# Kernel tuning notes

Measured on AMD Instinct MI355X. Metric: run time of the kernel, lower is better.

Reference implementation:

```python
import jax, jax.numpy as jnp
import numpy as np

N, IN_DIM, HID, HEADS, OUT = 4096, 512, 256, 2, 40
LN_EPS = 1e-5


def setup_inputs() -> dict:
    key = jax.random.key(0)
    ks = jax.random.split(key, 12)
    s_in = 1.0 / np.sqrt(IN_DIM)
    s_o = 1.0 / np.sqrt(2 * HID)
    adj = jax.random.randint(ks[0], (HEADS, N, N), 0, 2).astype(jnp.float32)
    h = jax.random.normal(ks[1], (N, IN_DIM), dtype=jnp.float32)
    Wq = jax.random.uniform(ks[2], (HEADS, IN_DIM, HID), minval=-s_in, maxval=s_in)
    bq = jax.random.uniform(ks[3], (HEADS, HID), minval=-s_in, maxval=s_in)
    Wk = jax.random.uniform(ks[4], (HEADS, IN_DIM, HID), minval=-s_in, maxval=s_in)
    bk = jax.random.uniform(ks[5], (HEADS, HID), minval=-s_in, maxval=s_in)
    Wv = jax.random.uniform(ks[6], (HEADS, IN_DIM, HID), minval=-s_in, maxval=s_in)
    bv = jax.random.uniform(ks[7], (HEADS, HID), minval=-s_in, maxval=s_in)
    Wo = jax.random.uniform(ks[8], (2 * HID, IN_DIM), minval=-s_o, maxval=s_o)
    bo = jax.random.uniform(ks[9], (IN_DIM,), minval=-s_o, maxval=s_o)
    gamma = jnp.ones((IN_DIM,), jnp.float32)
    beta = jnp.zeros((IN_DIM,), jnp.float32)
    Wp = jax.random.uniform(ks[10], (IN_DIM, OUT), minval=-s_in, maxval=s_in)
    bp = jax.random.uniform(ks[11], (OUT,), minval=-s_in, maxval=s_in)
    return dict(adj=adj, h=h, Wq=Wq, bq=bq, Wk=Wk, bk=bk, Wv=Wv, bv=bv,
                Wo=Wo, bo=bo, gamma=gamma, beta=beta, Wp=Wp, bp=bp)


def reference(adj, h, Wq, bq, Wk, bk, Wv, bv, Wo, bo, gamma, beta, Wp, bp):
    # Per-head projections, vectorized over the head axis. [H, N, D]
    Q = jnp.einsum('ni,hid->hnd', h, Wq) + bq[:, None, :]
    K = jnp.einsum('ni,hid->hnd', h, Wk) + bk[:, None, :]
    V = jnp.einsum('ni,hid->hnd', h, Wv) + bv[:, None, :]
    # Dense QK^T, elementwise-multiplied (not -inf masked) by per-head adjacency.
    scores = jnp.einsum('hnd,hmd->hnm', Q, K) * adj          # [H, N, N]
    attn = jax.nn.softmax(scores, axis=-1)
    X = jnp.einsum('hnm,hmd->hnd', attn, V)                  # [H, N, D]
    # cat([X0, X1], dim=1) -> [N, H*D]
    X_final = jnp.transpose(X, (1, 0, 2)).reshape(N, HEADS * HID)
    z = X_final @ Wo + bo                                    # [N, IN_DIM]
    mu = jnp.mean(z, axis=-1, keepdims=True)
    var = jnp.var(z, axis=-1, keepdims=True)
    M = (z - mu) * jax.lax.rsqrt(var + LN_EPS) * gamma + beta
    return jax.nn.softmax(M @ Wp + bp, axis=1)               # [N, OUT]
```

## Files before the change

kernel.cpp:

```cpp
#include <hip/hip_runtime.h>
#include <hip/hip_bf16.h>

#define N_TOK 4096
#define D_IN  512
#define D_HID 256
#define N_OUT 40

typedef _Float16 half8 __attribute__((ext_vector_type(8)));
typedef _Float16 half4 __attribute__((ext_vector_type(4)));
typedef float    f32x4 __attribute__((ext_vector_type(4)));

__device__ __forceinline__ void async_copy16(const _Float16* g, _Float16* l) {
  __builtin_amdgcn_global_load_lds(
      (const __attribute__((address_space(1))) unsigned int*)(g),
      (__attribute__((address_space(3))) unsigned int*)(l), 16, 0, 0);
}

__device__ __forceinline__ void transpose_tile(const float* __restrict__ src, int in_ncols,
                                               _Float16* __restrict__ dst, int out_ncols,
                                               int i0, int d0, float* lds )
{
  int tid = threadIdx.x;
  int l15 = tid & 15, l4 = tid >> 4;
#pragma unroll
  for (int p = 0; p < 4; p++) {
    int ii = p * 16 + l4;
    float4 x = *(const float4*)(src + (size_t)(i0 + ii) * in_ncols + d0 + l15 * 4);
    lds[(l15 * 4 + 0) * 65 + ii] = x.x;
    lds[(l15 * 4 + 1) * 65 + ii] = x.y;
    lds[(l15 * 4 + 2) * 65 + ii] = x.z;
    lds[(l15 * 4 + 3) * 65 + ii] = x.w;
  }
  __syncthreads();
  int dd = tid >> 2, chunk = tid & 3;
  half8 o0, o1;
#pragma unroll
  for (int j = 0; j < 8; j++) o0[j] = (_Float16)lds[dd * 65 + chunk * 16 + j];
#pragma unroll
  for (int j = 0; j < 8; j++) o1[j] = (_Float16)lds[dd * 65 + chunk * 16 + 8 + j];
  *(half8*)(dst + (size_t)(d0 + dd) * out_ncols + i0 + chunk * 16) = o0;
  *(half8*)(dst + (size_t)(d0 + dd) * out_ncols + i0 + chunk * 16 + 8) = o1;
}

__global__ void prep_kernel(const float* __restrict__ h, const float* __restrict__ Wq,
                            const float* __restrict__ Wk, const float* __restrict__ Wv,
                            const float* __restrict__ Wo, const float* __restrict__ Wp,
                            _Float16* __restrict__ h16, _Float16* __restrict__ Wqt,
                            _Float16* __restrict__ Wkt, _Float16* __restrict__ Wvt,
                            _Float16* __restrict__ Wot, _Float16* __restrict__ Wpt)
{
  __shared__ float lds[64 * 65];
  int b = blockIdx.x, tid = threadIdx.x;
  if (b < 1024) {
    int base = b * 2048 + tid * 8;
    float4 x0 = *(const float4*)(h + base);
    float4 x1 = *(const float4*)(h + base + 4);
    half8 o;
    o[0]=(_Float16)x0.x; o[1]=(_Float16)x0.y; o[2]=(_Float16)x0.z; o[3]=(_Float16)x0.w;
    o[4]=(_Float16)x1.x; o[5]=(_Float16)x1.y; o[6]=(_Float16)x1.z; o[7]=(_Float16)x1.w;
    *(half8*)(h16 + base) = o;
  } else if (b < 1216) {
    int t = b - 1024;
    int mat = t >> 5;
    int m = mat >> 1, head = mat & 1;
    const float* W = (m==0 ? Wq : (m==1 ? Wk : Wv)) + head * (D_IN * D_HID);
    _Float16* Wt   = (m==0 ? Wqt : (m==1 ? Wkt : Wvt)) + head * (D_IN * D_HID);
    int tt = t & 31;
    int i0 = (tt >> 2) * 64, d0 = (tt & 3) * 64;
    transpose_tile(W, D_HID, Wt, D_IN, i0, d0, lds);
  } else if (b < 1280) {
    int t = b - 1216;
    int i0 = (t >> 3) * 64, d0 = (t & 7) * 64;
    transpose_tile(Wo, D_IN, Wot, D_IN, i0, d0, lds);
  } else {
    int blk = b - 1280;
    int idx = blk * 1024 + tid * 4;
    int j = idx >> 9, i = idx & 511;
    half4 o;
#pragma unroll
    for (int u = 0; u < 4; u++)
      o[u] = (j < N_OUT) ? (_Float16)Wp[(i + u) * N_OUT + j] : (_Float16)0.f;
    *(half4*)(Wpt + j * D_IN + i) = o;
  }
}

__global__ __launch_bounds__(256, 2) void proj_kernel(
    const _Float16* __restrict__ h16, const _Float16* __restrict__ W6 ,
    const _Float16* __restrict__ Wvt,
    const float* __restrict__ bq, const float* __restrict__ bk,
    const float* __restrict__ bv,
    _Float16* __restrict__ Q16, _Float16* __restrict__ K16,
    _Float16* __restrict__ VT16)
{
  __shared__ __align__(16) _Float16 Atile[128 * 64];
  __shared__ __align__(16) _Float16 Btile[128 * 64];

  int b = blockIdx.x;
  int tid = threadIdx.x, w = tid >> 6, lane = tid & 63, quad = lane >> 4, cL = lane & 15;
  int wr = w >> 1, wc = w & 1;

  const _Float16 *Asrc, *Bsrc;
  int isV;
  int m0 = 0, n0 = 0, head = 0, mh = 0;
  if (b < 256) {
    isV = 0;
    m0 = (b >> 3) * 128;
    int ct = b & 7;
    mh = ct >> 1;
    n0 = (ct & 1) * 128;
    Asrc = h16 + (size_t)m0 * D_IN;
    Bsrc = W6 + (size_t)(ct * 128) * D_IN;
  } else {
    isV = 1;
    int t = b - 256;
    head = t >> 6;
    int tt = t & 63;
    m0 = (tt >> 5) * 128;
    n0 = (tt & 31) * 128;
    Asrc = Wvt + (size_t)head * (D_HID * D_IN) + (size_t)m0 * D_IN;
    Bsrc = h16 + (size_t)n0 * D_IN;
  }

  const f32x4 z4 = {0.f, 0.f, 0.f, 0.f};
  f32x4 acc[4][4];
#pragma unroll
  for (int i = 0; i < 4; i++)
#pragma unroll
    for (int j = 0; j < 4; j++) acc[i][j] = z4;

  int r8 = lane >> 3, chs = (lane & 7) ^ r8;

  for (int kc = 0; kc < 8; kc++) {
    __syncthreads();
#pragma unroll
    for (int g = 0; g < 4; g++) {
      int row = (w * 4 + g) * 8 + r8;
      async_copy16(Asrc + (size_t)row * D_IN + kc * 64 + chs * 8, Atile + (w * 4 + g) * 512);
      async_copy16(Bsrc + (size_t)row * D_IN + kc * 64 + chs * 8, Btile + (w * 4 + g) * 512);
    }
    __syncthreads();
#pragma unroll
    for (int kk = 0; kk < 2; kk++) {
      int ch = ((kk * 4 + quad) ^ (cL & 7)) * 8;
      half8 a[4], bf[4];
#pragma unroll
      for (int mt = 0; mt < 4; mt++)
        a[mt] = *(const half8*)(Atile + (wr * 64 + mt * 16 + cL) * 64 + ch);
#pragma unroll
      for (int nt = 0; nt < 4; nt++)
        bf[nt] = *(const half8*)(Btile + (wc * 64 + nt * 16 + cL) * 64 + ch);
#pragma unroll
      for (int mt = 0; mt < 4; mt++)
#pragma unroll
        for (int nt = 0; nt < 4; nt++)
          acc[mt][nt] = __builtin_amdgcn_mfma_f32_16x16x32_f16(a[mt], bf[nt], acc[mt][nt], 0, 0, 0);
    }
  }

  if (!isV) {
    _Float16* Out = (mh < 2 ? Q16 + (size_t)mh * (N_TOK * D_HID)
                            : K16 + (size_t)(mh - 2) * (N_TOK * D_HID));
    const float* bias = (mh < 2 ? bq + mh * D_HID : bk + (mh - 2) * D_HID);
#pragma unroll
    for (int mt = 0; mt < 4; mt++) {
      int row = m0 + wr * 64 + mt * 16 + quad * 4;
#pragma unroll
      for (int nt = 0; nt < 4; nt++) {
        int colg = n0 + wc * 64 + nt * 16 + cL;
        float bb = bias[colg];
#pragma unroll
        for (int reg = 0; reg < 4; reg++)
          Out[(size_t)(row + reg) * D_HID + colg] = (_Float16)(acc[mt][nt][reg] + bb);
      }
    }
  } else {
    _Float16* VTh = VT16 + (size_t)head * (N_TOK * D_HID);
    const float* bvh = bv + head * D_HID;
#pragma unroll
    for (int mt = 0; mt < 4; mt++) {
      int d0r = m0 + wr * 64 + mt * 16 + quad * 4;
      float bvv[4];
#pragma unroll
      for (int reg = 0; reg < 4; reg++) bvv[reg] = bvh[d0r + reg];
#pragma unroll
      for (int nt = 0; nt < 4; nt++) {
        int tok = n0 + wc * 64 + nt * 16 + cL;
#pragma unroll
        for (int reg = 0; reg < 4; reg++)
          VTh[(size_t)(d0r + reg) * N_TOK + tok] = (_Float16)(acc[mt][nt][reg] + bvv[reg]);
      }
    }
  }
}

__global__ __launch_bounds__(512, 2) void attn_kernel(
    const float* __restrict__ adj, const _Float16* __restrict__ Q16,
    const _Float16* __restrict__ K16, const _Float16* __restrict__ VT16,
    _Float16* __restrict__ Opart, float* __restrict__ Mpart, float* __restrict__ Lpart)
{
  __shared__ __align__(16) _Float16 Kt[2][64 * 256];
  __shared__ __align__(16) _Float16 Vt[2][256 * 64];
  __shared__ __align__(16) _Float16 Pbuf[8 * 16 * 72];

  int b = blockIdx.x;
  int head = (b >> 2) & 1;
  int gs = b & 3;
  int q0 = (b >> 3) * 128;

  int tid = threadIdx.x;
  int w = tid >> 6, lane = tid & 63, quad = lane >> 4, cL = lane & 15;

  const _Float16* Qh = Q16 + head * (N_TOK * D_HID);
  const _Float16* Kh = K16 + head * (N_TOK * D_HID);
  const _Float16* Vh = VT16 + head * (N_TOK * D_HID);
  const float* adjh = adj + (size_t)head * N_TOK * N_TOK;

  int qrow = q0 + w * 16;
  int nstart = gs * 1024;
  const f32x4 z4 = {0.f, 0.f, 0.f, 0.f};

  half8 qf[8];
#pragma unroll
  for (int t = 0; t < 8; t++)
    qf[t] = *(const half8*)(Qh + (qrow + cL) * D_HID + t * 32 + quad * 8);

  f32x4 acc[16];
#pragma unroll
  for (int i = 0; i < 16; i++) acc[i] = z4;
  float m_i[4] = {-1e30f, -1e30f, -1e30f, -1e30f};
  float l_i[4] = {0.f, 0.f, 0.f, 0.f};

  _Float16* pb = Pbuf + w * (16 * 72);

  const float* adjR[4];
#pragma unroll
  for (int reg = 0; reg < 4; reg++)
    adjR[reg] = adjh + (size_t)(qrow + quad * 4 + reg) * N_TOK + nstart + cL;

  int l5 = lane >> 5, l31 = lane & 31;
  int l3 = lane >> 3, l7 = lane & 7;

  auto stageK = [&](int it, _Float16* dst) {
    int n0 = nstart + it * 64;
#pragma unroll
    for (int i = 0; i < 4; i++) {
      int g = w * 4 + i;
      int rK = 2 * g + l5;
      int cK = l31 ^ (rK & 7);
      async_copy16(Kh + (size_t)(n0 + rK) * D_HID + cK * 8, dst + g * 512);
    }
  };
  auto stageV = [&](int it, _Float16* dst) {
    int n0 = nstart + it * 64;
#pragma unroll
    for (int i = 0; i < 4; i++) {
      int g = w * 4 + i;
      int rV = g * 8 + l3;
      int cV = l7 ^ (rV & 7);
      async_copy16(Vh + (size_t)rV * N_TOK + n0 + cV * 8, dst + g * 512);
    }
  };
  auto loadAdj = [&](int it, float (&av)[4][4]) {
#pragma unroll
    for (int reg = 0; reg < 4; reg++)
#pragma unroll
      for (int ct = 0; ct < 4; ct++)
        av[reg][ct] = __builtin_nontemporal_load(adjR[reg] + it * 64 + ct * 16);
  };

  auto body = [&](int it, const _Float16* KC, const _Float16* VC,
                  _Float16* KN, _Float16* VN,
                  float (&avC)[4][4], float (&avN)[4][4]) {
    if (it + 1 < 16) {
      stageK(it + 1, KN);
      stageV(it + 1, VN);
      loadAdj(it + 1, avN);
    }

    f32x4 s[4];
#pragma unroll
    for (int ct = 0; ct < 4; ct++) s[ct] = z4;
#pragma unroll
    for (int t = 0; t < 8; t++) {
#pragma unroll
      for (int ct = 0; ct < 4; ct++) {
        int rK = ct * 16 + cL;
        int ck = (t * 4 + quad) ^ (rK & 7);
        half8 kf = *(const half8*)(KC + rK * 256 + ck * 8);
        s[ct] = __builtin_amdgcn_mfma_f32_16x16x32_f16(qf[t], kf, s[ct], 0, 0, 0);
      }
    }

    float alpha[4];
#pragma unroll
    for (int reg = 0; reg < 4; reg++) {
#pragma unroll
      for (int ct = 0; ct < 4; ct++) s[ct][reg] *= avC[reg][ct];
      float mx = fmaxf(fmaxf(s[0][reg], s[1][reg]), fmaxf(s[2][reg], s[3][reg]));
#pragma unroll
      for (int msk = 1; msk < 16; msk <<= 1) mx = fmaxf(mx, __shfl_xor(mx, msk, 16));
      float mnew = fmaxf(m_i[reg], mx);
      alpha[reg] = __expf(m_i[reg] - mnew);
      m_i[reg] = mnew;
      float rs = 0.f;
#pragma unroll
      for (int ct = 0; ct < 4; ct++) {
        float p = __expf(s[ct][reg] - mnew);
        s[ct][reg] = p;
        rs += p;
      }
#pragma unroll
      for (int msk = 1; msk < 16; msk <<= 1) rs += __shfl_xor(rs, msk, 16);
      l_i[reg] = l_i[reg] * alpha[reg] + rs;
    }

#pragma unroll
    for (int reg = 0; reg < 4; reg++)
#pragma unroll
      for (int ct = 0; ct < 4; ct++)
        pb[(quad * 4 + reg) * 72 + ct * 16 + cL] = (_Float16)s[ct][reg];

    if (__any(alpha[0] * alpha[1] * alpha[2] * alpha[3] != 1.0f)) {
#pragma unroll
      for (int dt = 0; dt < 16; dt++)
#pragma unroll
        for (int reg = 0; reg < 4; reg++)
          acc[dt][reg] *= alpha[reg];
    }

    half8 pf0 = *(const half8*)(pb + cL * 72 + quad * 8);
    half8 pf1 = *(const half8*)(pb + cL * 72 + 32 + quad * 8);
#pragma unroll
    for (int dt = 0; dt < 16; dt++) {
      int rV = dt * 16 + cL;
      int c0 = (quad) ^ (rV & 7);
      int c1 = (4 + quad) ^ (rV & 7);
      half8 v0 = *(const half8*)(VC + rV * 64 + c0 * 8);
      half8 v1 = *(const half8*)(VC + rV * 64 + c1 * 8);
      acc[dt] = __builtin_amdgcn_mfma_f32_16x16x32_f16(pf0, v0, acc[dt], 0, 0, 0);
      acc[dt] = __builtin_amdgcn_mfma_f32_16x16x32_f16(pf1, v1, acc[dt], 0, 0, 0);
    }

    __syncthreads();
  };

  stageK(0, Kt[0]);
  stageV(0, Vt[0]);
  float avA[4][4], avB[4][4];
  loadAdj(0, avA);
  __syncthreads();

  for (int itp = 0; itp < 8; ++itp) {
    body(2 * itp,     Kt[0], Vt[0], Kt[1], Vt[1], avA, avB);
    body(2 * itp + 1, Kt[1], Vt[1], Kt[0], Vt[0], avB, avA);
  }

  int prow = (head * 4 + gs) * N_TOK + qrow + quad * 4;
#pragma unroll
  for (int reg = 0; reg < 4; reg++) {
    int row = prow + reg;
#pragma unroll
    for (int dt = 0; dt < 16; dt++)
      Opart[(size_t)row * D_HID + dt * 16 + cL] = (_Float16)acc[dt][reg];
    if (cL == 0) { Mpart[row] = m_i[reg]; Lpart[row] = l_i[reg]; }
  }
}

__global__ void merge_kernel(const _Float16* __restrict__ Opart,
                             const float* __restrict__ Mpart,
                             const float* __restrict__ Lpart,
                             _Float16* __restrict__ Xf)
{
  int t = blockIdx.x * 256 + threadIdx.x;
  int dg = (t & 63) << 2;
  int n = (t >> 6) & (N_TOK - 1);
  int head = t >> 18;
  int idx[4];
  float m[4], l[4];
  float mm = -1e30f;
#pragma unroll
  for (int s = 0; s < 4; s++) {
    idx[s] = (head * 4 + s) * N_TOK + n;
    m[s] = Mpart[idx[s]];
    l[s] = Lpart[idx[s]];
    mm = fmaxf(mm, m[s]);
  }
  float f[4], L = 0.f;
#pragma unroll
  for (int s = 0; s < 4; s++) { f[s] = __expf(m[s] - mm); L += f[s] * l[s]; }
  float rl = 1.0f / L;
  float o[4] = {0.f, 0.f, 0.f, 0.f};
#pragma unroll
  for (int s = 0; s < 4; s++) {
    half4 os = *(const half4*)(Opart + (size_t)idx[s] * D_HID + dg);
#pragma unroll
    for (int u = 0; u < 4; u++) o[u] += (float)os[u] * f[s];
  }
  half4 res;
#pragma unroll
  for (int u = 0; u < 4; u++) res[u] = (_Float16)(o[u] * rl);
  *(half4*)(Xf + (size_t)n * D_IN + head * D_HID + dg) = res;
}

__global__ __launch_bounds__(256, 1) void final_kernel(
    const _Float16* __restrict__ Xf, const _Float16* __restrict__ Wot,
    const _Float16* __restrict__ Wpt, const float* __restrict__ bo,
    const float* __restrict__ gamma, const float* __restrict__ beta,
    const float* __restrict__ bp, float* __restrict__ out)
{
  __shared__ __align__(16) _Float16 Btile[512 * 64];
  __shared__ __align__(16) _Float16 Mlds[16 * 520];
  __shared__ float outs[16 * 48];
  __shared__ float lnsum[4][16], lnsq[4][16];
  __shared__ float smx[16], srl[16];

  int rowbase = blockIdx.x * 16;
  int tid = threadIdx.x, w = tid >> 6, lane = tid & 63, quad = lane >> 4, cL = lane & 15;
  const f32x4 z4 = {0.f, 0.f, 0.f, 0.f};

  half8 af[16];
#pragma unroll
  for (int t = 0; t < 16; t++)
    af[t] = *(const half8*)(Xf + (rowbase + cL) * D_IN + t * 32 + quad * 8);

  f32x4 acc[8];
#pragma unroll
  for (int i = 0; i < 8; i++) acc[i] = z4;

  int r8 = lane >> 3, chs = (lane & 7) ^ r8;

  for (int kc = 0; kc < 8; kc++) {
    __syncthreads();
#pragma unroll
    for (int g = 0; g < 16; g++) {
      int row = (w * 16 + g) * 8 + r8;
      async_copy16(Wot + (size_t)row * D_IN + kc * 64 + chs * 8, Btile + (w * 16 + g) * 512);
    }
    __syncthreads();
#pragma unroll
    for (int kk = 0; kk < 2; kk++) {
      int ch = ((kk * 4 + quad) ^ (cL & 7)) * 8;
      half8 a = af[kc * 2 + kk];
      half8 bf[8];
#pragma unroll
      for (int nt = 0; nt < 8; nt++)
        bf[nt] = *(const half8*)(Btile + (w * 128 + nt * 16 + cL) * 64 + ch);
#pragma unroll
      for (int nt = 0; nt < 8; nt++)
        acc[nt] = __builtin_amdgcn_mfma_f32_16x16x32_f16(a, bf[nt], acc[nt], 0, 0, 0);
    }
  }

  float sum[4] = {0, 0, 0, 0}, sq[4] = {0, 0, 0, 0};
#pragma unroll
  for (int nt = 0; nt < 8; nt++) {
    int col = w * 128 + nt * 16 + cL;
    float bb = bo[col];
#pragma unroll
    for (int reg = 0; reg < 4; reg++) {
      float z = acc[nt][reg] + bb;
      acc[nt][reg] = z;
      sum[reg] += z;
      sq[reg] += z * z;
    }
  }
#pragma unroll
  for (int reg = 0; reg < 4; reg++) {
#pragma unroll
    for (int msk = 1; msk < 16; msk <<= 1) {
      sum[reg] += __shfl_xor(sum[reg], msk, 16);
      sq[reg]  += __shfl_xor(sq[reg], msk, 16);
    }
  }
  if (cL == 0) {
#pragma unroll
    for (int reg = 0; reg < 4; reg++) {
      lnsum[w][quad * 4 + reg] = sum[reg];
      lnsq[w][quad * 4 + reg]  = sq[reg];
    }
  }
  __syncthreads();
  float mean[4], rstd[4];
#pragma unroll
  for (int reg = 0; reg < 4; reg++) {
    int row = quad * 4 + reg;
    float s  = lnsum[0][row] + lnsum[1][row] + lnsum[2][row] + lnsum[3][row];
    float s2 = lnsq[0][row]  + lnsq[1][row]  + lnsq[2][row]  + lnsq[3][row];
    float mu = s * (1.0f / 512.0f);
    float var = s2 * (1.0f / 512.0f) - mu * mu;
    mean[reg] = mu;
    rstd[reg] = rsqrtf(var + 1e-5f);
  }
#pragma unroll
  for (int nt = 0; nt < 8; nt++) {
    int col = w * 128 + nt * 16 + cL;
    float g = gamma[col], be = beta[col];
#pragma unroll
    for (int reg = 0; reg < 4; reg++) {
      float mval = (acc[nt][reg] - mean[reg]) * rstd[reg] * g + be;
      Mlds[(quad * 4 + reg) * 520 + col] = (_Float16)mval;
    }
  }
  __syncthreads();
  if (w < 3) {
    int jt = w;
    f32x4 a2 = z4;
#pragma unroll
    for (int t = 0; t < 16; t++) {
      half8 am = *(const half8*)(Mlds + cL * 520 + t * 32 + quad * 8);
      half8 bm = *(const half8*)(Wpt + (jt * 16 + cL) * D_IN + t * 32 + quad * 8);
      a2 = __builtin_amdgcn_mfma_f32_16x16x32_f16(am, bm, a2, 0, 0, 0);
    }
    int col = jt * 16 + cL;
    float bpv = (col < N_OUT) ? bp[col] : 0.0f;
#pragma unroll
    for (int reg = 0; reg < 4; reg++)
      outs[(quad * 4 + reg) * 48 + col] = a2[reg] + bpv;
  }
  __syncthreads();
  if (tid < 16) {
    int row = tid;
    float mx = -1e30f;
    for (int j = 0; j < N_OUT; j++) mx = fmaxf(mx, outs[row * 48 + j]);
    float ssum = 0.f;
    for (int j = 0; j < N_OUT; j++) ssum += __expf(outs[row * 48 + j] - mx);
    smx[row] = mx;
    srl[row] = 1.0f / ssum;
  }
  __syncthreads();
#pragma unroll
  for (int i = 0; i < 3; i++) {
    int lin = tid + 256 * i;
    if (lin < 16 * N_OUT) {
      int row = lin / N_OUT, col = lin % N_OUT;
      out[(size_t)(rowbase + row) * N_OUT + col] =
          __expf(outs[row * 48 + col] - smx[row]) * srl[row];
    }
  }
}

#define OFF_WOT   0u
#define OFF_WPT   524288u
#define OFF_Q16   573440u
#define OFF_K16   4767744u
#define OFF_VT16  8962048u
#define OFF_MP    13156352u
#define OFF_LP    13287424u
#define OFF_XF    13418496u
#define OFF_OP    17612800u
#define OFF_H16   17612800u
#define OFF_WQT   21807104u
#define OFF_WKT   22331392u
#define OFF_WVT   22855680u

extern "C" void kernel_launch(void* const* d_in, const int* in_sizes, int n_in,
                              void* d_out, int out_size, void* d_ws, size_t ws_size,
                              hipStream_t stream)
{
  const float* adj   = (const float*)d_in[0];
  const float* h     = (const float*)d_in[1];
  const float* Wq    = (const float*)d_in[2];
  const float* bq    = (const float*)d_in[3];
  const float* Wk    = (const float*)d_in[4];
  const float* bk    = (const float*)d_in[5];
  const float* Wv    = (const float*)d_in[6];
  const float* bv    = (const float*)d_in[7];
  const float* Wo    = (const float*)d_in[8];
  const float* bo    = (const float*)d_in[9];
  const float* gamma = (const float*)d_in[10];
  const float* beta  = (const float*)d_in[11];
  const float* Wp    = (const float*)d_in[12];
  const float* bp    = (const float*)d_in[13];
  float* out = (float*)d_out;
  char* ws = (char*)d_ws;

  _Float16* h16   = (_Float16*)(ws + OFF_H16);
  _Float16* Wqt   = (_Float16*)(ws + OFF_WQT);
  _Float16* Wkt   = (_Float16*)(ws + OFF_WKT);
  _Float16* Wvt   = (_Float16*)(ws + OFF_WVT);
  _Float16* Wot   = (_Float16*)(ws + OFF_WOT);
  _Float16* Wpt   = (_Float16*)(ws + OFF_WPT);
  _Float16* Q16   = (_Float16*)(ws + OFF_Q16);
  _Float16* K16   = (_Float16*)(ws + OFF_K16);
  _Float16* VT16  = (_Float16*)(ws + OFF_VT16);
  _Float16* Opart = (_Float16*)(ws + OFF_OP);
  float*    Mpart = (float*)(ws + OFF_MP);
  float*    Lpart = (float*)(ws + OFF_LP);
  _Float16* Xf    = (_Float16*)(ws + OFF_XF);

  prep_kernel<<<1304, 256, 0, stream>>>(h, Wq, Wk, Wv, Wo, Wp,
                                        h16, Wqt, Wkt, Wvt, Wot, Wpt);
  proj_kernel<<<384, 256, 0, stream>>>(h16, Wqt, Wvt, bq, bk, bv,
                                       Q16, K16, VT16);
  attn_kernel<<<256, 512, 0, stream>>>(adj, Q16, K16, VT16, Opart, Mpart, Lpart);
  merge_kernel<<<2048, 256, 0, stream>>>(Opart, Mpart, Lpart, Xf);
  final_kernel<<<256, 256, 0, stream>>>(Xf, Wot, Wpt, bo, gamma, beta, bp, out);
}
```

Baseline: 302.4 us.

## Fuse split-KV merge into final kernel and raise MFMA wave priority

Removes the separate merge kernel by having the final kernel combine the four partial attention outputs with their max/sum statistics while loading its A fragments, which drops one launch and the Xf round trip through global memory. It also wraps the QK and PV MFMA loops in the attention kernel with s_setprio so matrix-issuing waves are favoured over waves doing softmax or loads. The fused load reads four partial rows per fragment inside a 256-block kernel, which may expose more latency there.

```diff
diff --git a/kernel.cpp b/kernel.cpp
--- a/kernel.cpp
+++ b/kernel.cpp
@@ -280,6 +280,7 @@
     f32x4 s[4];
 #pragma unroll
     for (int ct = 0; ct < 4; ct++) s[ct] = z4;
+    __builtin_amdgcn_s_setprio(1);
 #pragma unroll
     for (int t = 0; t < 8; t++) {
 #pragma unroll
@@ -290,6 +291,7 @@
         s[ct] = __builtin_amdgcn_mfma_f32_16x16x32_f16(qf[t], kf, s[ct], 0, 0, 0);
       }
     }
+    __builtin_amdgcn_s_setprio(0);
 
     float alpha[4];
 #pragma unroll
@@ -330,6 +332,7 @@
 
     half8 pf0 = *(const half8*)(pb + cL * 72 + quad * 8);
     half8 pf1 = *(const half8*)(pb + cL * 72 + 32 + quad * 8);
+    __builtin_amdgcn_s_setprio(1);
 #pragma unroll
     for (int dt = 0; dt < 16; dt++) {
       int rV = dt * 16 + cL;
@@ -340,6 +343,7 @@
       acc[dt] = __builtin_amdgcn_mfma_f32_16x16x32_f16(pf0, v0, acc[dt], 0, 0, 0);
       acc[dt] = __builtin_amdgcn_mfma_f32_16x16x32_f16(pf1, v1, acc[dt], 0, 0, 0);
     }
+    __builtin_amdgcn_s_setprio(0);
 
     __syncthreads();
   };
@@ -366,44 +370,9 @@
   }
 }
 
-__global__ void merge_kernel(const _Float16* __restrict__ Opart,
-                             const float* __restrict__ Mpart,
-                             const float* __restrict__ Lpart,
-                             _Float16* __restrict__ Xf)
-{
-  int t = blockIdx.x * 256 + threadIdx.x;
-  int dg = (t & 63) << 2;
-  int n = (t >> 6) & (N_TOK - 1);
-  int head = t >> 18;
-  int idx[4];
-  float m[4], l[4];
-  float mm = -1e30f;
-#pragma unroll
-  for (int s = 0; s < 4; s++) {
-    idx[s] = (head * 4 + s) * N_TOK + n;
-    m[s] = Mpart[idx[s]];
-    l[s] = Lpart[idx[s]];
-    mm = fmaxf(mm, m[s]);
-  }
-  float f[4], L = 0.f;
-#pragma unroll
-  for (int s = 0; s < 4; s++) { f[s] = __expf(m[s] - mm); L += f[s] * l[s]; }
-  float rl = 1.0f / L;
-  float o[4] = {0.f, 0.f, 0.f, 0.f};
-#pragma unroll
-  for (int s = 0; s < 4; s++) {
-    half4 os = *(const half4*)(Opart + (size_t)idx[s] * D_HID + dg);
-#pragma unroll
-    for (int u = 0; u < 4; u++) o[u] += (float)os[u] * f[s];
-  }
-  half4 res;
-#pragma unroll
-  for (int u = 0; u < 4; u++) res[u] = (_Float16)(o[u] * rl);
-  *(half4*)(Xf + (size_t)n * D_IN + head * D_HID + dg) = res;
-}
-
 __global__ __launch_bounds__(256, 1) void final_kernel(
-    const _Float16* __restrict__ Xf, const _Float16* __restrict__ Wot,
+    const _Float16* __restrict__ Opart, const float* __restrict__ Mpart,
+    const float* __restrict__ Lpart, const _Float16* __restrict__ Wot,
     const _Float16* __restrict__ Wpt, const float* __restrict__ bo,
     const float* __restrict__ gamma, const float* __restrict__ beta,
     const float* __restrict__ bp, float* __restrict__ out)
@@ -417,11 +386,43 @@
   int rowbase = blockIdx.x * 16;
   int tid = threadIdx.x, w = tid >> 6, lane = tid & 63, quad = lane >> 4, cL = lane & 15;
   const f32x4 z4 = {0.f, 0.f, 0.f, 0.f};
+  int row = rowbase + cL;
+
+  float fr[2][4];
+#pragma unroll
+  for (int hd = 0; hd < 2; hd++) {
+    float m[4], l[4];
+    float mm = -1e30f;
+#pragma unroll
+    for (int s = 0; s < 4; s++) {
+      int idx = (hd * 4 + s) * N_TOK + row;
+      m[s] = Mpart[idx];
+      l[s] = Lpart[idx];
+      mm = fmaxf(mm, m[s]);
+    }
+    float f_[4], L = 0.f;
+#pragma unroll
+    for (int s = 0; s < 4; s++) { f_[s] = __expf(m[s] - mm); L += f_[s] * l[s]; }
+    float rl = 1.0f / L;
+#pragma unroll
+    for (int s = 0; s < 4; s++) fr[hd][s] = f_[s] * rl;
+  }
 
   half8 af[16];
 #pragma unroll
-  for (int t = 0; t < 16; t++)
-    af[t] = *(const half8*)(Xf + (rowbase + cL) * D_IN + t * 32 + quad * 8);
+  for (int t = 0; t < 16; t++) {
+    int hd = t >> 3;
+    int dg = (t & 7) * 32 + quad * 8;
+    float o[8] = {0.f, 0.f, 0.f, 0.f, 0.f, 0.f, 0.f, 0.f};
+#pragma unroll
+    for (int s = 0; s < 4; s++) {
+      half8 os = *(const half8*)(Opart + (size_t)((hd * 4 + s) * N_TOK + row) * D_HID + dg);
+#pragma unroll
+      for (int u = 0; u < 8; u++) o[u] += (float)os[u] * fr[hd][s];
+    }
+#pragma unroll
+    for (int u = 0; u < 8; u++) af[t][u] = (_Float16)o[u];
+  }
 
   f32x4 acc[8];
 #pragma unroll
@@ -433,8 +434,8 @@
     __syncthreads();
 #pragma unroll
     for (int g = 0; g < 16; g++) {
-      int row = (w * 16 + g) * 8 + r8;
-      async_copy16(Wot + (size_t)row * D_IN + kc * 64 + chs * 8, Btile + (w * 16 + g) * 512);
+      int grow = (w * 16 + g) * 8 + r8;
+      async_copy16(Wot + (size_t)grow * D_IN + kc * 64 + chs * 8, Btile + (w * 16 + g) * 512);
     }
     __syncthreads();
 #pragma unroll
@@ -483,9 +484,9 @@
   float mean[4], rstd[4];
 #pragma unroll
   for (int reg = 0; reg < 4; reg++) {
-    int row = quad * 4 + reg;
-    float s  = lnsum[0][row] + lnsum[1][row] + lnsum[2][row] + lnsum[3][row];
-    float s2 = lnsq[0][row]  + lnsq[1][row]  + lnsq[2][row]  + lnsq[3][row];
+    int r = quad * 4 + reg;
+    float s  = lnsum[0][r] + lnsum[1][r] + lnsum[2][r] + lnsum[3][r];
+    float s2 = lnsq[0][r]  + lnsq[1][r]  + lnsq[2][r]  + lnsq[3][r];
     float mu = s * (1.0f / 512.0f);
     float var = s2 * (1.0f / 512.0f) - mu * mu;
     mean[reg] = mu;
@@ -519,22 +520,22 @@
   }
   __syncthreads();
   if (tid < 16) {
-    int row = tid;
+    int r = tid;
     float mx = -1e30f;
-    for (int j = 0; j < N_OUT; j++) mx = fmaxf(mx, outs[row * 48 + j]);
+    for (int j = 0; j < N_OUT; j++) mx = fmaxf(mx, outs[r * 48 + j]);
     float ssum = 0.f;
-    for (int j = 0; j < N_OUT; j++) ssum += __expf(outs[row * 48 + j] - mx);
-    smx[row] = mx;
-    srl[row] = 1.0f / ssum;
+    for (int j = 0; j < N_OUT; j++) ssum += __expf(outs[r * 48 + j] - mx);
+    smx[r] = mx;
+    srl[r] = 1.0f / ssum;
   }
   __syncthreads();
 #pragma unroll
   for (int i = 0; i < 3; i++) {
     int lin = tid + 256 * i;
     if (lin < 16 * N_OUT) {
-      int row = lin / N_OUT, col = lin % N_OUT;
-      out[(size_t)(rowbase + row) * N_OUT + col] =
-          __expf(outs[row * 48 + col] - smx[row]) * srl[row];
+      int r = lin / N_OUT, col = lin % N_OUT;
+      out[(size_t)(rowbase + r) * N_OUT + col] =
+          __expf(outs[r * 48 + col] - smx[r]) * srl[r];
     }
   }
 }
@@ -546,7 +547,6 @@
 #define OFF_VT16  8962048u
 #define OFF_MP    13156352u
 #define OFF_LP    13287424u
-#define OFF_XF    13418496u
 #define OFF_OP    17612800u
 #define OFF_H16   17612800u
 #define OFF_WQT   21807104u
@@ -586,13 +586,12 @@
   _Float16* Opart = (_Float16*)(ws + OFF_OP);
   float*    Mpart = (float*)(ws + OFF_MP);
   float*    Lpart = (float*)(ws + OFF_LP);
-  _Float16* Xf    = (_Float16*)(ws + OFF_XF);
 
   prep_kernel<<<1304, 256, 0, stream>>>(h, Wq, Wk, Wv, Wo, Wp,
                                         h16, Wqt, Wkt, Wvt, Wot, Wpt);
   proj_kernel<<<384, 256, 0, stream>>>(h16, Wqt, Wvt, bq, bk, bv,
                                        Q16, K16, VT16);
   attn_kernel<<<256, 512, 0, stream>>>(adj, Q16, K16, VT16, Opart, Mpart, Lpart);
-  merge_kernel<<<2048, 256, 0, stream>>>(Opart, Mpart, Lpart, Xf);
-  final_kernel<<<256, 256, 0, stream>>>(Xf, Wot, Wpt, bo, gamma, beta, bp, out);
-}
+  final_kernel<<<256, 256, 0, stream>>>(Opart, Mpart, Lpart, Wot, Wpt,
+                                        bo, gamma, beta, bp, out);
+}
```

New measurement: 306.4 us. Within noise of the previous version (+1.3%).
